# Optimization experiments

Hardware: AMD Instinct MI355X
Metric: run time of the kernel (lower is better)

## Reference

```python
import jax, jax.numpy as jnp
import numpy as np

B, T, C, H = 4, 2048, 1024, 16  # batch, seq, embed, heads; head_dim = C // H = 64


def setup_inputs() -> dict:
    key = jax.random.key(0)
    ks = jax.random.split(key, 9)
    s = 1.0 / np.sqrt(C)
    return {
        "query": jax.random.normal(ks[0], (B, T, C), jnp.float32),
        "key": jax.random.normal(ks[1], (B, T, C), jnp.float32),
        "value": jax.random.normal(ks[2], (B, T, C), jnp.float32),
        "mask": jax.random.randint(ks[3], (1, 1, T, T), 0, 2, jnp.int32),
        "Wq": jax.random.normal(ks[4], (C, C), jnp.float32) * s,
        "Wk": jax.random.normal(ks[5], (C, C), jnp.float32) * s,
        "Wv": jax.random.normal(ks[6], (C, C), jnp.float32) * s,
        "Wp": jax.random.normal(ks[7], (C, C), jnp.float32) * s,
        "bp": jax.random.normal(ks[8], (C,), jnp.float32) * s,
    }


def reference(query, key, value, mask, Wq, Wk, Wv, Wp, bp):
    # torch Linear: y = x @ W.T (no bias for q/k/v)
    q = jnp.einsum("btc,dc->btd", query, Wq)
    k = jnp.einsum("btc,dc->btd", key, Wk)
    v = jnp.einsum("btc,dc->btd", value, Wv)
    hd = C // H
    # [B,T,C] -> [B,H,T,hd]
    q = q.reshape(B, T, H, hd).transpose(0, 2, 1, 3)
    k = k.reshape(B, T, H, hd).transpose(0, 2, 1, 3)
    v = v.reshape(B, T, H, hd).transpose(0, 2, 1, 3)
    # NOTE: scale uses FULL embed dim C (faithful to source), not head_dim.
    wei = jnp.einsum("bhqd,bhkd->bhqk", q, k) * (C ** -0.5)
    # Faithful quirk: masked positions are zero-filled (not -inf) BEFORE softmax.
    wei = jnp.where(mask == 0, jnp.zeros((), wei.dtype), wei)
    wei = jax.nn.softmax(wei, axis=-1)
    out = jnp.einsum("bhqk,bhkd->bhqd", wei, v)
    out = out.transpose(0, 2, 1, 3).reshape(B, T, C)
    # proj (dropout omitted: eval mode / p=0)
    return jnp.einsum("btc,dc->btd", out, Wp) + bp
```

## Files before the change

kernel.cpp:

```cpp
#include <hip/hip_runtime.h>
#include <hip/hip_bf16.h>
#include <cstdint>
#include <cstddef>

static constexpr int Bn = 4, Tn = 2048, Cn = 1024, Hn = 16, HD = 64;
static constexpr int Mn = Bn * Tn;
static constexpr float QSCALE = 0.03125f * 1.4426950408889634f;

typedef __attribute__((ext_vector_type(8))) short s16x8;
typedef __attribute__((ext_vector_type(4))) short s16x4;
typedef __attribute__((ext_vector_type(4))) float f32x4;
typedef __attribute__((ext_vector_type(2))) unsigned u32x2;

#define DEVFN __device__ __forceinline__

DEVFN unsigned short f2bf(float f) {
  union { float f; unsigned u; } v; v.f = f;
  unsigned r = v.u + 0x7fffu + ((v.u >> 16) & 1u);
  return (unsigned short)(r >> 16);
}

DEVFN float exp2_hw(float x) {
  float r;
  asm("v_exp_f32 %0, %1" : "=v"(r) : "v"(x));
  return r;
}

DEVFN void gload_lds16(const void* g, void* l) {
  __builtin_amdgcn_global_load_lds(
      (const __attribute__((address_space(1))) void*)g,
      (__attribute__((address_space(3))) void*)l, 16, 0, 0);
}

__global__ __launch_bounds__(256) void k_prep(
    const float* __restrict__ q, const float* __restrict__ k, const float* __restrict__ v,
    const float* __restrict__ wq, const float* __restrict__ wk,
    const float* __restrict__ wv, const float* __restrict__ wp,
    const int* __restrict__ mask,
    unsigned short* __restrict__ Xq, unsigned short* __restrict__ Xk,
    unsigned short* __restrict__ Xv,
    unsigned short* __restrict__ Wqb, unsigned short* __restrict__ Wkb,
    unsigned short* __restrict__ Wvb, unsigned short* __restrict__ Wpb,
    unsigned* __restrict__ bits) {
  const int NX = (Mn * Cn / 4) / 256;
  const int NW = (Cn * Cn / 4) / 256;
  int bid = blockIdx.x, tid = threadIdx.x;
  if (bid < 3 * NX) {
    const float* src = bid < NX ? q : (bid < 2 * NX ? k : v);
    unsigned short* dst = bid < NX ? Xq : (bid < 2 * NX ? Xk : Xv);
    int i = (bid & (NX - 1)) * 256 + tid;
    float4 vv = reinterpret_cast<const float4*>(src)[i];
    ushort4 o;
    o.x = f2bf(vv.x); o.y = f2bf(vv.y); o.z = f2bf(vv.z); o.w = f2bf(vv.w);
    reinterpret_cast<ushort4*>(dst)[i] = o;
  } else if (bid < 3 * NX + 4 * NW) {
    int t = (bid - 3 * NX) / NW;
    const float* src = t == 0 ? wq : t == 1 ? wk : t == 2 ? wv : wp;
    unsigned short* dst = t == 0 ? Wqb : t == 1 ? Wkb : t == 2 ? Wvb : Wpb;
    int i = ((bid - 3 * NX) & (NW - 1)) * 256 + tid;
    float4 vv = reinterpret_cast<const float4*>(src)[i];
    ushort4 o;
    o.x = f2bf(vv.x); o.y = f2bf(vv.y); o.z = f2bf(vv.z); o.w = f2bf(vv.w);
    reinterpret_cast<ushort4*>(dst)[i] = o;
  } else {
    int i = (bid - 3 * NX - 4 * NW) * 256 + tid;
    unsigned long long b = __ballot(mask[i] != 0);
    int lane = tid & 63;
    if (lane == 0)        bits[i >> 5] = (unsigned)b;
    else if (lane == 32)  bits[i >> 5] = (unsigned)(b >> 32);
  }
}

template <bool F32OUT>
DEVFN void gemm_body(const unsigned short* __restrict__ A,
                     const unsigned short* __restrict__ Bt,
                     void* __restrict__ Cv, const float* __restrict__ bias,
                     float oscale, int bx, int by) {
  const int N = Cn, K = Cn;
  __shared__ __align__(16) char As[128 * 64 * 2];
  __shared__ __align__(16) char Bs[128 * 64 * 2];
  const int tid = threadIdx.x, lane = tid & 63, wid = tid >> 6;
  const int l15 = lane & 15, lg = lane >> 4;
  const int wm = (wid >> 1) * 64, wn = (wid & 1) * 64;
  const int m0 = by * 128, n0 = bx * 128;

  f32x4 acc[4][4];
#pragma unroll
  for (int i = 0; i < 4; ++i)
#pragma unroll
    for (int j = 0; j < 4; ++j) acc[i][j] = f32x4{0.f, 0.f, 0.f, 0.f};

  for (int k0 = 0; k0 < K; k0 += 64) {
#pragma unroll
    for (int it = 0; it < 4; ++it) {
      int chunk = it * 256 + tid;
      int row = chunk >> 3;
      int kg = (chunk & 7) ^ (row & 7);
      gload_lds16(A + (size_t)(m0 + row) * K + k0 + kg * 8,
                  As + (it * 256 + wid * 64) * 16);
      gload_lds16(Bt + (size_t)(n0 + row) * K + k0 + kg * 8,
                  Bs + (it * 256 + wid * 64) * 16);
    }
    __syncthreads();
#pragma unroll
    for (int kk = 0; kk < 64; kk += 32) {
      s16x8 a[4], b[4];
#pragma unroll
      for (int i = 0; i < 4; ++i) {
        int ra = wm + i * 16 + l15;
        a[i] = *(const s16x8*)(As + ra * 128 + (((kk + lg * 8) * 2) ^ ((ra & 7) << 4)));
        int rb = wn + i * 16 + l15;
        b[i] = *(const s16x8*)(Bs + rb * 128 + (((kk + lg * 8) * 2) ^ ((rb & 7) << 4)));
      }
#pragma unroll
      for (int i = 0; i < 4; ++i)
#pragma unroll
        for (int j = 0; j < 4; ++j)
          acc[i][j] = __builtin_amdgcn_mfma_f32_16x16x32_bf16(a[i], b[j], acc[i][j], 0, 0, 0);
    }
    __syncthreads();
  }
#pragma unroll
  for (int i = 0; i < 4; ++i)
#pragma unroll
    for (int j = 0; j < 4; ++j)
#pragma unroll
      for (int q = 0; q < 4; ++q) {
        int r = m0 + wm + i * 16 + lg * 4 + q;
        int c = n0 + wn + j * 16 + l15;
        float v = acc[i][j][q];
        if (F32OUT) ((float*)Cv)[(size_t)r * N + c] = v + bias[c];
        else        ((unsigned short*)Cv)[(size_t)r * N + c] = f2bf(v * oscale);
      }
}

DEVFN void gemm_swz(int& bx, int& by) {
  int flat = blockIdx.y * 8 + blockIdx.x;
  int swz = (flat & 7) * 64 + (flat >> 3);
  bx = swz & 7; by = swz >> 3;
}

__global__ __launch_bounds__(256) void k_gemmQKV(
    const unsigned short* __restrict__ Xq, const unsigned short* __restrict__ Xk,
    const unsigned short* __restrict__ Xv,
    const unsigned short* __restrict__ Wqb, const unsigned short* __restrict__ Wkb,
    const unsigned short* __restrict__ Wvb,
    unsigned short* __restrict__ Qb, unsigned short* __restrict__ Kb,
    unsigned short* __restrict__ Vb) {
  int z = blockIdx.z;
  const unsigned short* A  = z == 0 ? Xq : z == 1 ? Xk : Xv;
  const unsigned short* Bt = z == 0 ? Wqb : z == 1 ? Wkb : Wvb;
  unsigned short* C        = z == 0 ? Qb : z == 1 ? Kb : Vb;
  float oscale             = z == 0 ? QSCALE : 1.0f;
  int bx, by; gemm_swz(bx, by);
  gemm_body<false>(A, Bt, C, nullptr, oscale, bx, by);
}

__global__ __launch_bounds__(256) void k_gemmO(const unsigned short* __restrict__ A,
                                               const unsigned short* __restrict__ Bt,
                                               float* __restrict__ C,
                                               const float* __restrict__ bias) {
  int bx, by; gemm_swz(bx, by);
  gemm_body<true>(A, Bt, C, bias, 1.0f, bx, by);
}

__global__ __launch_bounds__(256) void k_attn(const unsigned short* __restrict__ Qg,
                                              const unsigned short* __restrict__ Kg,
                                              const unsigned short* __restrict__ Vg,
                                              const unsigned* __restrict__ mbits,
                                              unsigned short* __restrict__ Og) {
  __shared__ __align__(16) char QPs[128 * 128];
  __shared__ __align__(16) char Ks[64 * 128];
  __shared__ __align__(16) char Vts[64 * 128];
  __shared__ unsigned Mw[128 * 2];
  __shared__ float Ls[128];

  const int tid = threadIdx.x, lane = tid & 63, wid = tid >> 6;
  const int l15 = lane & 15, lg = lane >> 4;
  const int qt = blockIdx.x, bh = blockIdx.y;
  const int b = bh >> 4, h = bh & 15;
  const size_t rowbase = (size_t)b * Tn;
  const int cbase = h * 64;

  const int dp = lane & 31;
  const int g  = wid * 2 + (lane >> 5);
  const int qrm = tid >> 1, wmi = tid & 1;

#pragma unroll
  for (int it = 0; it < 4; ++it) {
    int chunk = it * 256 + tid;
    int row = chunk >> 3;
    int kg = (chunk & 7) ^ (row & 7);
    gload_lds16(Qg + (rowbase + qt * 128 + row) * Cn + cbase + kg * 8,
                QPs + (it * 256 + wid * 64) * 16);
  }
#pragma unroll
  for (int it = 0; it < 2; ++it) {
    int chunk = it * 256 + tid;
    int row = chunk >> 3;
    int kg = (chunk & 7) ^ (row & 7);
    gload_lds16(Kg + (rowbase + row) * Cn + cbase + kg * 8,
                Ks + (it * 256 + wid * 64) * 16);
  }
  unsigned w[8];
  {
    const unsigned* vsrc = (const unsigned*)(Vg + (rowbase + g * 8) * Cn + cbase) + dp;
#pragma unroll
    for (int j = 0; j < 8; ++j) w[j] = vsrc[(size_t)j * (Cn / 2)];
  }
  unsigned mreg = mbits[(size_t)(qt * 128 + qrm) * (Tn / 32) + wmi];
  __syncthreads();

  s16x8 qf[2][2];
#pragma unroll
  for (int m = 0; m < 2; ++m)
#pragma unroll
    for (int kh = 0; kh < 2; ++kh) {
      int ra = wid * 32 + m * 16 + l15;
      qf[m][kh] = *(const s16x8*)(QPs + ra * 128 + ((kh * 64 + lg * 16) ^ ((ra & 7) << 4)));
    }
  {
    union { unsigned u[4]; s16x8 v; } lo, hi;
#pragma unroll
    for (int j = 0; j < 4; ++j) {
      lo.u[j] = __builtin_amdgcn_perm(w[2 * j + 1], w[2 * j], 0x05040100u);
      hi.u[j] = __builtin_amdgcn_perm(w[2 * j + 1], w[2 * j], 0x07060302u);
    }
    int d0 = dp * 2, swv = (dp & 7) << 4;
    *(s16x8*)(Vts + d0 * 128 + ((g * 16) ^ swv)) = lo.v;
    *(s16x8*)(Vts + (d0 + 1) * 128 + ((g * 16) ^ swv)) = hi.v;
    Mw[qrm * 2 + wmi] = mreg;
  }

  f32x4 oacc[2][4];
#pragma unroll
  for (int m = 0; m < 2; ++m)
#pragma unroll
    for (int n = 0; n < 4; ++n) oacc[m][n] = f32x4{0.f, 0.f, 0.f, 0.f};
  float lsum[2] = {0.0f, 0.0f};

  char* Pw = QPs + wid * (32 * 128);

  for (int kt = 0; kt < Tn / 64; ++kt) {
    f32x4 sacc[4][2];
#pragma unroll
    for (int n = 0; n < 4; ++n)
#pragma unroll
      for (int m = 0; m < 2; ++m) sacc[n][m] = f32x4{0.f, 0.f, 0.f, 0.f};
#pragma unroll
    for (int kk = 0; kk < 64; kk += 32) {
      s16x8 kfr[4];
#pragma unroll
      for (int n = 0; n < 4; ++n) {
        int rb = n * 16 + l15;
        kfr[n] = *(const s16x8*)(Ks + rb * 128 + (((kk + lg * 8) * 2) ^ ((rb & 7) << 4)));
      }
#pragma unroll
      for (int n = 0; n < 4; ++n)
#pragma unroll
        for (int m = 0; m < 2; ++m)
          sacc[n][m] = __builtin_amdgcn_mfma_f32_16x16x32_bf16(kfr[n], qf[m][kk >> 5],
                                                               sacc[n][m], 0, 0, 0);
    }
    __syncthreads();

    {
      int ktn = (kt + 1) & (Tn / 64 - 1);
#pragma unroll
      for (int it = 0; it < 2; ++it) {
        int chunk = it * 256 + tid;
        int row = chunk >> 3;
        int kg = (chunk & 7) ^ (row & 7);
        gload_lds16(Kg + (rowbase + ktn * 64 + row) * Cn + cbase + kg * 8,
                    Ks + (it * 256 + wid * 64) * 16);
      }
      const unsigned* vsrc =
          (const unsigned*)(Vg + (rowbase + ktn * 64 + g * 8) * Cn + cbase) + dp;
#pragma unroll
      for (int j = 0; j < 8; ++j) w[j] = vsrc[(size_t)j * (Cn / 2)];
      mreg = mbits[(size_t)(qt * 128 + qrm) * (Tn / 32) + ktn * 2 + wmi];
    }

#pragma unroll
    for (int qi = 0; qi < 2; ++qi) {
      int qr = wid * 32 + qi * 16 + l15;
      unsigned w0 = Mw[qr * 2], w1 = Mw[qr * 2 + 1];
      int qloc = qi * 16 + l15;
      unsigned swp = (unsigned)((qloc & 7) << 4);
      float psum = 0.0f;
#pragma unroll
      for (int kf = 0; kf < 4; ++kf) {
        unsigned wm_ = (kf < 2) ? w0 : w1;
        unsigned bits4 = wm_ >> ((kf & 1) * 16 + lg * 4);
        unsigned pb[4];
#pragma unroll
        for (int r = 0; r < 4; ++r) {
          int smear = (int)(bits4 << (31 - r)) >> 31;
          union { float f; unsigned u; } sv; sv.f = sacc[kf][qi][r];
          sv.u &= (unsigned)smear;
          float pv = exp2_hw(sv.f);
          psum += pv;
          union { float f; unsigned u; } pc; pc.f = pv; pb[r] = pc.u;
        }
        union { u32x2 u; s16x4 s; } pk;
        pk.u.x = __builtin_amdgcn_perm(pb[1], pb[0], 0x07060302u);
        pk.u.y = __builtin_amdgcn_perm(pb[3], pb[2], 0x07060302u);
        *(s16x4*)(Pw + qloc * 128 + (((unsigned)(kf * 32 + lg * 8)) ^ swp)) = pk.s;
      }
      lsum[qi] += psum;
    }
    asm volatile("" ::: "memory");

#pragma unroll
    for (int kk = 0; kk < 64; kk += 32) {
      s16x8 pa[2], vb[4];
#pragma unroll
      for (int m = 0; m < 2; ++m) {
        int rp = m * 16 + l15;
        pa[m] = *(const s16x8*)(Pw + rp * 128 + (((kk + lg * 8) * 2) ^ ((rp & 7) << 4)));
      }
#pragma unroll
      for (int n = 0; n < 4; ++n) {
        int rv = n * 16 + l15;
        vb[n] = *(const s16x8*)(Vts + rv * 128 + (((kk + lg * 8) * 2) ^ (((rv >> 1) & 7) << 4)));
      }
#pragma unroll
      for (int m = 0; m < 2; ++m)
#pragma unroll
        for (int n = 0; n < 4; ++n)
          oacc[m][n] = __builtin_amdgcn_mfma_f32_16x16x32_bf16(pa[m], vb[n], oacc[m][n], 0, 0, 0);
    }
    __syncthreads();

    {
      union { unsigned u[4]; s16x8 v; } lo, hi;
#pragma unroll
      for (int j = 0; j < 4; ++j) {
        lo.u[j] = __builtin_amdgcn_perm(w[2 * j + 1], w[2 * j], 0x05040100u);
        hi.u[j] = __builtin_amdgcn_perm(w[2 * j + 1], w[2 * j], 0x07060302u);
      }
      int d0 = dp * 2, swv = (dp & 7) << 4;
      *(s16x8*)(Vts + d0 * 128 + ((g * 16) ^ swv)) = lo.v;
      *(s16x8*)(Vts + (d0 + 1) * 128 + ((g * 16) ^ swv)) = hi.v;
      Mw[qrm * 2 + wmi] = mreg;
    }
  }

#pragma unroll
  for (int qi = 0; qi < 2; ++qi) {
    float v = lsum[qi];
    v += __shfl_xor(v, 16);
    v += __shfl_xor(v, 32);
    if (lg == 0) Ls[wid * 32 + qi * 16 + l15] = v;
  }
  asm volatile("" ::: "memory");

#pragma unroll
  for (int m = 0; m < 2; ++m)
#pragma unroll
    for (int q = 0; q < 4; ++q) {
      int rloc = wid * 32 + m * 16 + lg * 4 + q;
      float inv = 1.0f / Ls[rloc];
      int rg = qt * 128 + rloc;
#pragma unroll
      for (int n = 0; n < 4; ++n)
        Og[(rowbase + rg) * Cn + cbase + n * 16 + l15] = f2bf(oacc[m][n][q] * inv);
    }
}

extern "C" void kernel_launch(void* const* d_in, const int* in_sizes, int n_in,
                              void* d_out, int out_size, void* d_ws, size_t ws_size,
                              hipStream_t stream) {
  (void)in_sizes; (void)n_in; (void)out_size; (void)ws_size;
  const float* query = (const float*)d_in[0];
  const float* key_  = (const float*)d_in[1];
  const float* value = (const float*)d_in[2];
  const int*   mask  = (const int*)d_in[3];
  const float* Wq = (const float*)d_in[4];
  const float* Wk = (const float*)d_in[5];
  const float* Wv = (const float*)d_in[6];
  const float* Wp = (const float*)d_in[7];
  const float* bp = (const float*)d_in[8];

  char* ws = (char*)d_ws;
  const size_t SX = (size_t)Mn * Cn * 2;
  const size_t SW = (size_t)Cn * Cn * 2;
  unsigned short* Xq  = (unsigned short*)(ws);
  unsigned short* Xk  = (unsigned short*)(ws + SX);
  unsigned short* Xv  = (unsigned short*)(ws + 2 * SX);
  unsigned short* Wqb = (unsigned short*)(ws + 3 * SX);
  unsigned short* Wkb = (unsigned short*)(ws + 3 * SX + SW);
  unsigned short* Wvb = (unsigned short*)(ws + 3 * SX + 2 * SW);
  unsigned short* Wpb = (unsigned short*)(ws + 3 * SX + 3 * SW);
  unsigned short* Qb  = (unsigned short*)(ws + 3 * SX + 4 * SW);
  unsigned short* Kb  = (unsigned short*)(ws + 4 * SX + 4 * SW);
  unsigned short* Vb  = (unsigned short*)(ws + 5 * SX + 4 * SW);
  unsigned*       mb  = (unsigned*)(ws + 6 * SX + 4 * SW);
  unsigned short* AO  = Xq;

  const int NPREP = 3 * ((Mn * Cn / 4) / 256) + 4 * ((Cn * Cn / 4) / 256)
                    + (Tn * Tn) / 256;
  k_prep<<<dim3(NPREP), dim3(256), 0, stream>>>(query, key_, value, Wq, Wk, Wv, Wp, mask,
                                                Xq, Xk, Xv, Wqb, Wkb, Wvb, Wpb, mb);

  k_gemmQKV<<<dim3(8, 64, 3), dim3(256), 0, stream>>>(Xq, Xk, Xv, Wqb, Wkb, Wvb,
                                                      Qb, Kb, Vb);

  k_attn<<<dim3(16, 64), dim3(256), 0, stream>>>(Qb, Kb, Vb, mb, AO);

  k_gemmO<<<dim3(8, 64), dim3(256), 0, stream>>>(AO, Wpb, (float*)d_out, bp);
}
```

Before: 224.9 us.

## Double-buffer K, V and mask tiles in attention to drop a barrier per tile

The attention loop now keeps two LDS buffers each for K, transposed V and mask words. The next tile's loads are issued into the alternate buffer at the start of each iteration, and the loop body is unrolled by two so the buffers swap roles. This removes one of the two __syncthreads per key tile and lets global loads overlap the QK and PV MFMA work. In exchange it adds about 17 KB of extra LDS per block, which may lower occupancy.

```diff
diff --git a/kernel.cpp b/kernel.cpp
--- a/kernel.cpp
+++ b/kernel.cpp
@@ -164,34 +164,160 @@
   gemm_body<true>(A, Bt, C, bias, 1.0f, bx, by);
 }
 
+struct AttnCtx {
+  const unsigned short* Kg;
+  const unsigned short* Vg;
+  const unsigned* mbits;
+  size_t rowbase;
+  int cbase, qt;
+  int tid, lane, wid, l15, lg, dp, g, qrm, wmi;
+};
+
+DEVFN void attn_tile(const AttnCtx& C, int kt,
+                     char* Kcur, char* Knxt, char* Vcur, char* Vnxt,
+                     unsigned* Mcur, unsigned* Mnxt,
+                     char* Pw, const s16x8 qf[2][2],
+                     f32x4 oacc[2][4], float lsum[2]) {
+  const int l15 = C.l15, lg = C.lg, wid = C.wid, tid = C.tid;
+  int ktn = (kt + 1) & (Tn / 64 - 1);
+  unsigned w[8];
+  {
+#pragma unroll
+    for (int it = 0; it < 2; ++it) {
+      int chunk = it * 256 + tid;
+      int row = chunk >> 3;
+      int kg = (chunk & 7) ^ (row & 7);
+      gload_lds16(C.Kg + (C.rowbase + ktn * 64 + row) * Cn + C.cbase + kg * 8,
+                  Knxt + (it * 256 + wid * 64) * 16);
+    }
+    const unsigned* vsrc =
+        (const unsigned*)(C.Vg + (C.rowbase + ktn * 64 + C.g * 8) * Cn + C.cbase) + C.dp;
+#pragma unroll
+    for (int j = 0; j < 8; ++j) w[j] = vsrc[(size_t)j * (Cn / 2)];
+  }
+  unsigned mreg = C.mbits[(size_t)(C.qt * 128 + C.qrm) * (Tn / 32) + ktn * 2 + C.wmi];
+
+  f32x4 sacc[4][2];
+#pragma unroll
+  for (int n = 0; n < 4; ++n)
+#pragma unroll
+    for (int m = 0; m < 2; ++m) sacc[n][m] = f32x4{0.f, 0.f, 0.f, 0.f};
+#pragma unroll
+  for (int kk = 0; kk < 64; kk += 32) {
+    s16x8 kfr[4];
+#pragma unroll
+    for (int n = 0; n < 4; ++n) {
+      int rb = n * 16 + l15;
+      kfr[n] = *(const s16x8*)(Kcur + rb * 128 + (((kk + lg * 8) * 2) ^ ((rb & 7) << 4)));
+    }
+#pragma unroll
+    for (int n = 0; n < 4; ++n)
+#pragma unroll
+      for (int m = 0; m < 2; ++m)
+        sacc[n][m] = __builtin_amdgcn_mfma_f32_16x16x32_bf16(kfr[n], qf[m][kk >> 5],
+                                                             sacc[n][m], 0, 0, 0);
+  }
+
+#pragma unroll
+  for (int qi = 0; qi < 2; ++qi) {
+    int qr = wid * 32 + qi * 16 + l15;
+    unsigned w0 = Mcur[qr * 2], w1 = Mcur[qr * 2 + 1];
+    int qloc = qi * 16 + l15;
+    unsigned swp = (unsigned)((qloc & 7) << 4);
+    float psum = 0.0f;
+#pragma unroll
+    for (int kf = 0; kf < 4; ++kf) {
+      unsigned wm_ = (kf < 2) ? w0 : w1;
+      unsigned bits4 = wm_ >> ((kf & 1) * 16 + lg * 4);
+      unsigned pb[4];
+#pragma unroll
+      for (int r = 0; r < 4; ++r) {
+        int smear = (int)(bits4 << (31 - r)) >> 31;
+        union { float f; unsigned u; } sv; sv.f = sacc[kf][qi][r];
+        sv.u &= (unsigned)smear;
+        float pv = exp2_hw(sv.f);
+        psum += pv;
+        union { float f; unsigned u; } pc; pc.f = pv; pb[r] = pc.u;
+      }
+      union { u32x2 u; s16x4 s; } pk;
+      pk.u.x = __builtin_amdgcn_perm(pb[1], pb[0], 0x07060302u);
+      pk.u.y = __builtin_amdgcn_perm(pb[3], pb[2], 0x07060302u);
+      *(s16x4*)(Pw + qloc * 128 + (((unsigned)(kf * 32 + lg * 8)) ^ swp)) = pk.s;
+    }
+    lsum[qi] += psum;
+  }
+  asm volatile("" ::: "memory");
+
+#pragma unroll
+  for (int kk = 0; kk < 64; kk += 32) {
+    s16x8 pa[2], vb[4];
+#pragma unroll
+    for (int m = 0; m < 2; ++m) {
+      int rp = m * 16 + l15;
+      pa[m] = *(const s16x8*)(Pw + rp * 128 + (((kk + lg * 8) * 2) ^ ((rp & 7) << 4)));
+    }
+#pragma unroll
+    for (int n = 0; n < 4; ++n) {
+      int rv = n * 16 + l15;
+      vb[n] = *(const s16x8*)(Vcur + rv * 128 + (((kk + lg * 8) * 2) ^ (((rv >> 1) & 7) << 4)));
+    }
+#pragma unroll
+    for (int m = 0; m < 2; ++m)
+#pragma unroll
+      for (int n = 0; n < 4; ++n)
+        oacc[m][n] = __builtin_amdgcn_mfma_f32_16x16x32_bf16(pa[m], vb[n], oacc[m][n], 0, 0, 0);
+  }
+
+  {
+    union { unsigned u[4]; s16x8 v; } lo, hi;
+#pragma unroll
+    for (int j = 0; j < 4; ++j) {
+      lo.u[j] = __builtin_amdgcn_perm(w[2 * j + 1], w[2 * j], 0x05040100u);
+      hi.u[j] = __builtin_amdgcn_perm(w[2 * j + 1], w[2 * j], 0x07060302u);
+    }
+    int d0 = C.dp * 2, swv = (C.dp & 7) << 4;
+    *(s16x8*)(Vnxt + d0 * 128 + ((C.g * 16) ^ swv)) = lo.v;
+    *(s16x8*)(Vnxt + (d0 + 1) * 128 + ((C.g * 16) ^ swv)) = hi.v;
+    Mnxt[C.qrm * 2 + C.wmi] = mreg;
+  }
+  __syncthreads();
+}
+
 __global__ __launch_bounds__(256) void k_attn(const unsigned short* __restrict__ Qg,
                                               const unsigned short* __restrict__ Kg,
                                               const unsigned short* __restrict__ Vg,
                                               const unsigned* __restrict__ mbits,
                                               unsigned short* __restrict__ Og) {
   __shared__ __align__(16) char QPs[128 * 128];
-  __shared__ __align__(16) char Ks[64 * 128];
-  __shared__ __align__(16) char Vts[64 * 128];
-  __shared__ unsigned Mw[128 * 2];
+  __shared__ __align__(16) char Ks0[64 * 128];
+  __shared__ __align__(16) char Ks1[64 * 128];
+  __shared__ __align__(16) char Vt0[64 * 128];
+  __shared__ __align__(16) char Vt1[64 * 128];
+  __shared__ unsigned Mw0[128 * 2];
+  __shared__ unsigned Mw1[128 * 2];
   __shared__ float Ls[128];
 
-  const int tid = threadIdx.x, lane = tid & 63, wid = tid >> 6;
-  const int l15 = lane & 15, lg = lane >> 4;
-  const int qt = blockIdx.x, bh = blockIdx.y;
-  const int b = bh >> 4, h = bh & 15;
-  const size_t rowbase = (size_t)b * Tn;
-  const int cbase = h * 64;
-
-  const int dp = lane & 31;
-  const int g  = wid * 2 + (lane >> 5);
-  const int qrm = tid >> 1, wmi = tid & 1;
+  AttnCtx C;
+  C.Kg = Kg; C.Vg = Vg; C.mbits = mbits;
+  C.tid = threadIdx.x; C.lane = C.tid & 63; C.wid = C.tid >> 6;
+  C.l15 = C.lane & 15; C.lg = C.lane >> 4;
+  C.qt = blockIdx.x;
+  int bh = blockIdx.y;
+  int b = bh >> 4, h = bh & 15;
+  C.rowbase = (size_t)b * Tn;
+  C.cbase = h * 64;
+  C.dp = C.lane & 31;
+  C.g  = C.wid * 2 + (C.lane >> 5);
+  C.qrm = C.tid >> 1; C.wmi = C.tid & 1;
+
+  const int tid = C.tid, wid = C.wid, l15 = C.l15, lg = C.lg;
 
 #pragma unroll
   for (int it = 0; it < 4; ++it) {
     int chunk = it * 256 + tid;
     int row = chunk >> 3;
     int kg = (chunk & 7) ^ (row & 7);
-    gload_lds16(Qg + (rowbase + qt * 128 + row) * Cn + cbase + kg * 8,
+    gload_lds16(Qg + (C.rowbase + C.qt * 128 + row) * Cn + C.cbase + kg * 8,
                 QPs + (it * 256 + wid * 64) * 16);
   }
 #pragma unroll
@@ -199,16 +325,16 @@
     int chunk = it * 256 + tid;
     int row = chunk >> 3;
     int kg = (chunk & 7) ^ (row & 7);
-    gload_lds16(Kg + (rowbase + row) * Cn + cbase + kg * 8,
-                Ks + (it * 256 + wid * 64) * 16);
+    gload_lds16(Kg + (C.rowbase + row) * Cn + C.cbase + kg * 8,
+                Ks0 + (it * 256 + wid * 64) * 16);
   }
   unsigned w[8];
   {
-    const unsigned* vsrc = (const unsigned*)(Vg + (rowbase + g * 8) * Cn + cbase) + dp;
+    const unsigned* vsrc = (const unsigned*)(Vg + (C.rowbase + C.g * 8) * Cn + C.cbase) + C.dp;
 #pragma unroll
     for (int j = 0; j < 8; ++j) w[j] = vsrc[(size_t)j * (Cn / 2)];
   }
-  unsigned mreg = mbits[(size_t)(qt * 128 + qrm) * (Tn / 32) + wmi];
+  unsigned mreg = mbits[(size_t)(C.qt * 128 + C.qrm) * (Tn / 32) + C.wmi];
   __syncthreads();
 
   s16x8 qf[2][2];
@@ -226,11 +352,12 @@
       lo.u[j] = __builtin_amdgcn_perm(w[2 * j + 1], w[2 * j], 0x05040100u);
       hi.u[j] = __builtin_amdgcn_perm(w[2 * j + 1], w[2 * j], 0x07060302u);
     }
-    int d0 = dp * 2, swv = (dp & 7) << 4;
-    *(s16x8*)(Vts + d0 * 128 + ((g * 16) ^ swv)) = lo.v;
-    *(s16x8*)(Vts + (d0 + 1) * 128 + ((g * 16) ^ swv)) = hi.v;
-    Mw[qrm * 2 + wmi] = mreg;
-  }
+    int d0 = C.dp * 2, swv = (C.dp & 7) << 4;
+    *(s16x8*)(Vt0 + d0 * 128 + ((C.g * 16) ^ swv)) = lo.v;
+    *(s16x8*)(Vt0 + (d0 + 1) * 128 + ((C.g * 16) ^ swv)) = hi.v;
+    Mw0[C.qrm * 2 + C.wmi] = mreg;
+  }
+  __syncthreads();
 
   f32x4 oacc[2][4];
 #pragma unroll
@@ -241,109 +368,9 @@
 
   char* Pw = QPs + wid * (32 * 128);
 
-  for (int kt = 0; kt < Tn / 64; ++kt) {
-    f32x4 sacc[4][2];
-#pragma unroll
-    for (int n = 0; n < 4; ++n)
-#pragma unroll
-      for (int m = 0; m < 2; ++m) sacc[n][m] = f32x4{0.f, 0.f, 0.f, 0.f};
-#pragma unroll
-    for (int kk = 0; kk < 64; kk += 32) {
-      s16x8 kfr[4];
-#pragma unroll
-      for (int n = 0; n < 4; ++n) {
-        int rb = n * 16 + l15;
-        kfr[n] = *(const s16x8*)(Ks + rb * 128 + (((kk + lg * 8) * 2) ^ ((rb & 7) << 4)));
-      }
-#pragma unroll
-      for (int n = 0; n < 4; ++n)
-#pragma unroll
-        for (int m = 0; m < 2; ++m)
-          sacc[n][m] = __builtin_amdgcn_mfma_f32_16x16x32_bf16(kfr[n], qf[m][kk >> 5],
-                                                               sacc[n][m], 0, 0, 0);
-    }
-    __syncthreads();
-
-    {
-      int ktn = (kt + 1) & (Tn / 64 - 1);
-#pragma unroll
-      for (int it = 0; it < 2; ++it) {
-        int chunk = it * 256 + tid;
-        int row = chunk >> 3;
-        int kg = (chunk & 7) ^ (row & 7);
-        gload_lds16(Kg + (rowbase + ktn * 64 + row) * Cn + cbase + kg * 8,
-                    Ks + (it * 256 + wid * 64) * 16);
-      }
-      const unsigned* vsrc =
-          (const unsigned*)(Vg + (rowbase + ktn * 64 + g * 8) * Cn + cbase) + dp;
-#pragma unroll
-      for (int j = 0; j < 8; ++j) w[j] = vsrc[(size_t)j * (Cn / 2)];
-      mreg = mbits[(size_t)(qt * 128 + qrm) * (Tn / 32) + ktn * 2 + wmi];
-    }
-
-#pragma unroll
-    for (int qi = 0; qi < 2; ++qi) {
-      int qr = wid * 32 + qi * 16 + l15;
-      unsigned w0 = Mw[qr * 2], w1 = Mw[qr * 2 + 1];
-      int qloc = qi * 16 + l15;
-      unsigned swp = (unsigned)((qloc & 7) << 4);
-      float psum = 0.0f;
-#pragma unroll
-      for (int kf = 0; kf < 4; ++kf) {
-        unsigned wm_ = (kf < 2) ? w0 : w1;
-        unsigned bits4 = wm_ >> ((kf & 1) * 16 + lg * 4);
-        unsigned pb[4];
-#pragma unroll
-        for (int r = 0; r < 4; ++r) {
-          int smear = (int)(bits4 << (31 - r)) >> 31;
-          union { float f; unsigned u; } sv; sv.f = sacc[kf][qi][r];
-          sv.u &= (unsigned)smear;
-          float pv = exp2_hw(sv.f);
-          psum += pv;
-          union { float f; unsigned u; } pc; pc.f = pv; pb[r] = pc.u;
-        }
-        union { u32x2 u; s16x4 s; } pk;
-        pk.u.x = __builtin_amdgcn_perm(pb[1], pb[0], 0x07060302u);
-        pk.u.y = __builtin_amdgcn_perm(pb[3], pb[2], 0x07060302u);
-        *(s16x4*)(Pw + qloc * 128 + (((unsigned)(kf * 32 + lg * 8)) ^ swp)) = pk.s;
-      }
-      lsum[qi] += psum;
-    }
-    asm volatile("" ::: "memory");
-
-#pragma unroll
-    for (int kk = 0; kk < 64; kk += 32) {
-      s16x8 pa[2], vb[4];
-#pragma unroll
-      for (int m = 0; m < 2; ++m) {
-        int rp = m * 16 + l15;
-        pa[m] = *(const s16x8*)(Pw + rp * 128 + (((kk + lg * 8) * 2) ^ ((rp & 7) << 4)));
-      }
-#pragma unroll
-      for (int n = 0; n < 4; ++n) {
-        int rv = n * 16 + l15;
-        vb[n] = *(const s16x8*)(Vts + rv * 128 + (((kk + lg * 8) * 2) ^ (((rv >> 1) & 7) << 4)));
-      }
-#pragma unroll
-      for (int m = 0; m < 2; ++m)
-#pragma unroll
-        for (int n = 0; n < 4; ++n)
-          oacc[m][n] = __builtin_amdgcn_mfma_f32_16x16x32_bf16(pa[m], vb[n], oacc[m][n], 0, 0, 0);
-    }
-    __syncthreads();
-
-    {
-      union { unsigned u[4]; s16x8 v; } lo, hi;
-#pragma unroll
-      for (int j = 0; j < 4; ++j) {
-        lo.u[j] = __builtin_amdgcn_perm(w[2 * j + 1], w[2 * j], 0x05040100u);
-        hi.u[j] = __builtin_amdgcn_perm(w[2 * j + 1], w[2 * j], 0x07060302u);
-      }
-      int d0 = dp * 2, swv = (dp & 7) << 4;
-      *(s16x8*)(Vts + d0 * 128 + ((g * 16) ^ swv)) = lo.v;
-      *(s16x8*)(Vts + (d0 + 1) * 128 + ((g * 16) ^ swv)) = hi.v;
-      Mw[qrm * 2 + wmi] = mreg;
-    }
+  for (int kt2 = 0; kt2 < Tn / 128; ++kt2) {
+    attn_tile(C, kt2 * 2,     Ks0, Ks1, Vt0, Vt1, Mw0, Mw1, Pw, qf, oacc, lsum);
+    attn_tile(C, kt2 * 2 + 1, Ks1, Ks0, Vt1, Vt0, Mw1, Mw0, Pw, qf, oacc, lsum);
   }
 
 #pragma unroll
@@ -361,10 +388,10 @@
     for (int q = 0; q < 4; ++q) {
       int rloc = wid * 32 + m * 16 + lg * 4 + q;
       float inv = 1.0f / Ls[rloc];
-      int rg = qt * 128 + rloc;
+      int rg = C.qt * 128 + rloc;
 #pragma unroll
       for (int n = 0; n < 4; ++n)
-        Og[(rowbase + rg) * Cn + cbase + n * 16 + l15] = f2bf(oacc[m][n][q] * inv);
+        Og[(C.rowbase + rg) * Cn + C.cbase + n * 16 + l15] = f2bf(oacc[m][n][q] * inv);
     }
 }
 
```

Measured after the change: 232.2 us. +3.2%, slower.
